# Optimization experiments

Hardware: AMD Instinct MI355X
Metric: run time of the kernel (lower is better)

## Reference

```python
import jax, jax.numpy as jnp
import numpy as np

D = 1024        # hidden_dim
E = 8           # num_experts
K = 2           # activated_experts
H = 4 * D       # ffn hidden


def setup_inputs() -> dict:
    key = jax.random.key(0)
    ks = jax.random.split(key, 12)
    s = 1.0 / np.sqrt(D)
    sh = 1.0 / np.sqrt(H)
    return {
        "x": jax.random.normal(ks[0], (2, 2048, D), dtype=jnp.float32),
        "gate_w": jax.random.uniform(ks[1], (D, E), minval=-s, maxval=s, dtype=jnp.float32),
        "gate_b": jax.random.uniform(ks[2], (E,), minval=-s, maxval=s, dtype=jnp.float32),
        "route_bias": jnp.zeros((E,), dtype=jnp.float32),
        "shared_w1": jax.random.uniform(ks[3], (D, H), minval=-s, maxval=s, dtype=jnp.float32),
        "shared_b1": jax.random.uniform(ks[4], (H,), minval=-s, maxval=s, dtype=jnp.float32),
        "shared_w2": jax.random.uniform(ks[5], (H, D), minval=-sh, maxval=sh, dtype=jnp.float32),
        "shared_b2": jax.random.uniform(ks[6], (D,), minval=-sh, maxval=sh, dtype=jnp.float32),
        "exp_w1": jax.random.uniform(ks[7], (E, D, H), minval=-s, maxval=s, dtype=jnp.float32),
        "exp_b1": jax.random.uniform(ks[8], (E, H), minval=-s, maxval=s, dtype=jnp.float32),
        "exp_w2": jax.random.uniform(ks[9], (E, H, D), minval=-sh, maxval=sh, dtype=jnp.float32),
        "exp_b2": jax.random.uniform(ks[10], (E, D), minval=-sh, maxval=sh, dtype=jnp.float32),
    }


def reference(x, gate_w, gate_b, route_bias, shared_w1, shared_b1, shared_w2,
              shared_b2, exp_w1, exp_b1, exp_w2, exp_b2):
    B, S, _ = x.shape
    xf = x.reshape(-1, D)                                  # [T, D]
    T = xf.shape[0]

    # Routing: gate logits + learned load-balancing bias -> softmax -> top-k
    gate_logits = xf @ gate_w + gate_b + route_bias        # [T, E]
    gate_probs = jax.nn.softmax(gate_logits, axis=-1)
    topk_p, topk_i = jax.lax.top_k(gate_probs, K)          # [T, K]
    topk_p = topk_p / jnp.sum(topk_p, axis=-1, keepdims=True)

    # Per-token combine weights over experts (zero for unselected experts)
    w = jnp.zeros((T, E), dtype=xf.dtype)
    w = w.at[jnp.arange(T)[:, None], topk_i].add(topk_p)   # [T, E]

    # Dense per-expert FFN (grouped GEMM form), weighted combine
    h = jax.nn.gelu(jnp.einsum('td,edh->eth', xf, exp_w1) + exp_b1[:, None, :],
                    approximate=False)                     # [E, T, H]
    y = jnp.einsum('eth,ehd->etd', h, exp_w2) + exp_b2[:, None, :]  # [E, T, D]
    combined = jnp.einsum('etd,te->td', y, w)              # [T, D]

    # Shared expert
    sh = jax.nn.gelu(xf @ shared_w1 + shared_b1, approximate=False)
    shared_out = sh @ shared_w2 + shared_b2                # [T, D]

    return (shared_out + combined).reshape(B, S, D)
```

## Files before the change

kernel.cpp:

```cpp
#include <hip/hip_runtime.h>
#include <math.h>

#define TT 4096
#define DD 1024
#define EE 8
#define HH 4096
#define NEXP 9

typedef __bf16 bf16;
typedef __bf16 bf16x8 __attribute__((ext_vector_type(8)));
typedef float  f32x4  __attribute__((ext_vector_type(4)));

#define GLOAD_LDS16(gptr, lptr)                                                   \
  __builtin_amdgcn_global_load_lds(                                               \
      (const __attribute__((address_space(1))) void*)(gptr),                      \
      (__attribute__((address_space(3))) void*)(lptr), 16, 0, 0)

__global__ void k_init(const float* __restrict__ x, bf16* __restrict__ xb,
                       float* __restrict__ out, int* __restrict__ counts,
                       int* __restrict__ cursors) {
  int i = blockIdx.x * blockDim.x + threadIdx.x;
  if (i < TT * DD) { xb[i] = (bf16)x[i]; out[i] = 0.0f; }
  if (i < EE) { counts[i] = 0; cursors[i] = 0; }
}

__global__ void k_route(const float* __restrict__ x, const float* __restrict__ gw,
                        const float* __restrict__ gb, const float* __restrict__ rb,
                        int* __restrict__ counts, int* __restrict__ tke,
                        float* __restrict__ tkp) {
  int gid = blockIdx.x * blockDim.x + threadIdx.x;
  int t = gid >> 6;
  int lane = gid & 63;
  if (t >= TT) return;
  const float* xt = x + (size_t)t * DD;
  float acc[EE];
#pragma unroll
  for (int e = 0; e < EE; e++) acc[e] = 0.f;
  for (int d = lane; d < DD; d += 64) {
    float xv = xt[d];
    const float* g = gw + (size_t)d * EE;
#pragma unroll
    for (int e = 0; e < EE; e++) acc[e] += xv * g[e];
  }
#pragma unroll
  for (int off = 32; off > 0; off >>= 1) {
#pragma unroll
    for (int e = 0; e < EE; e++) acc[e] += __shfl_down(acc[e], off);
  }
  if (lane == 0) {
    float l[EE];
#pragma unroll
    for (int e = 0; e < EE; e++) l[e] = acc[e] + gb[e] + rb[e];
    int i1 = 0;
#pragma unroll
    for (int e = 1; e < EE; e++) if (l[e] > l[i1]) i1 = e;
    int i2 = (i1 == 0) ? 1 : 0;
#pragma unroll
    for (int e = 0; e < EE; e++) if (e != i1 && l[e] > l[i2]) i2 = e;
    float e2 = expf(l[i2] - l[i1]);
    float s = 1.f + e2;
    tke[t * 2 + 0] = i1; tkp[t * 2 + 0] = 1.f / s;
    tke[t * 2 + 1] = i2; tkp[t * 2 + 1] = e2 / s;
    atomicAdd(&counts[i1], 1);
    atomicAdd(&counts[i2], 1);
  }
}

__global__ void k_prefix(const int* __restrict__ counts, int* __restrict__ expBase,
                         int* __restrict__ expCnt) {
  if (blockIdx.x == 0 && threadIdx.x == 0) {
    int off = TT;
    for (int e = 0; e < EE; e++) { expBase[e] = off; expCnt[e] = counts[e]; off += counts[e]; }
    expBase[8] = 0; expCnt[8] = TT;
  }
}

__global__ void k_scatter(const int* __restrict__ tke, const float* __restrict__ tkp,
                          const int* __restrict__ expBase, int* __restrict__ cursors,
                          int* __restrict__ rowTok, float* __restrict__ rowW) {
  int t = blockIdx.x * blockDim.x + threadIdx.x;
  if (t >= TT) return;
  rowTok[t] = t; rowW[t] = 1.f;
#pragma unroll
  for (int k = 0; k < 2; k++) {
    int e = tke[t * 2 + k];
    float p = tkp[t * 2 + k];
    int slot = atomicAdd(&cursors[e], 1);
    int r = expBase[e] + slot;
    rowTok[r] = t; rowW[r] = p;
  }
}

__global__ __launch_bounds__(256) void k_wt(const float* __restrict__ expW,
                                            const float* __restrict__ shW,
                                            bf16* __restrict__ outT, int K, int N) {
  __shared__ float t[64][65];
  int z = blockIdx.z;
  const float* W = (z == 8) ? shW : expW + (size_t)z * K * N;
  bf16* O = outT + (size_t)z * K * N;
  int n0 = blockIdx.x * 64, k0 = blockIdx.y * 64;
  int tid = threadIdx.x;
  int kr = tid >> 2;
  int cf = (tid & 3) * 16;
#pragma unroll
  for (int i = 0; i < 4; i++) {
    f32x4 v = *(const f32x4*)&W[(size_t)(k0 + kr) * N + n0 + cf + i * 4];
    t[kr][cf + i * 4 + 0] = v[0];
    t[kr][cf + i * 4 + 1] = v[1];
    t[kr][cf + i * 4 + 2] = v[2];
    t[kr][cf + i * 4 + 3] = v[3];
  }
  __syncthreads();
  int nr = tid >> 2;
  int kf = (tid & 3) * 16;
  bf16x8 o0, o1;
#pragma unroll
  for (int j = 0; j < 8; j++) o0[j] = (bf16)t[kf + j][nr];
#pragma unroll
  for (int j = 0; j < 8; j++) o1[j] = (bf16)t[kf + 8 + j][nr];
  bf16* dst = O + (size_t)(n0 + nr) * K + k0 + kf;
  *(bf16x8*)dst = o0;
  *(bf16x8*)(dst + 8) = o1;
}

__global__ __launch_bounds__(256, 2) void k_gemm1(
    const bf16* __restrict__ xb, const bf16* __restrict__ wt1,
    const float* __restrict__ sb1, const float* __restrict__ eb1,
    const int* __restrict__ rowTok, const int* __restrict__ expBase,
    const int* __restrict__ expCnt, bf16* __restrict__ hbuf) {
  int ex = blockIdx.z;
  int base = expBase[ex];
  int cnt  = expCnt[ex];
  int mt = blockIdx.y;
  if (mt * 128 >= cnt) return;
  int n0 = blockIdx.x * 128;
  const bf16* Bt = wt1 + (size_t)ex * HH * DD;
  const float* b1 = (ex == 8) ? sb1 : eb1 + (size_t)ex * HH;

  __shared__ bf16 As[128 * 32];
  __shared__ bf16 Bs[128 * 32];
  __shared__ int  toks[128];

  int tid = threadIdx.x;
  int lane = tid & 63;
  int wv = tid >> 6;
  int wm = (wv & 1) * 64;
  int wn = (wv >> 1) * 64;

  if (tid < 128) {
    int rr = min(mt * 128 + tid, cnt - 1);
    toks[tid] = rowTok[base + rr];
  }

  f32x4 acc[4][4];
#pragma unroll
  for (int a = 0; a < 4; a++)
#pragma unroll
    for (int b = 0; b < 4; b++) acc[a][b] = (f32x4){0.f, 0.f, 0.f, 0.f};

  __syncthreads();

  int r0 = wv * 32 + (lane >> 2);
  int c8 = (lane & 3) * 8;

  for (int k0 = 0; k0 < DD; k0 += 32) {
    GLOAD_LDS16(xb + (size_t)toks[r0] * DD + k0 + c8,      As + wv * 1024);
    GLOAD_LDS16(xb + (size_t)toks[r0 + 16] * DD + k0 + c8, As + wv * 1024 + 512);
    GLOAD_LDS16(Bt + (size_t)(n0 + r0) * DD + k0 + c8,      Bs + wv * 1024);
    GLOAD_LDS16(Bt + (size_t)(n0 + r0 + 16) * DD + k0 + c8, Bs + wv * 1024 + 512);
    __syncthreads();
    bf16x8 af[4], bfr[4];
#pragma unroll
    for (int mi = 0; mi < 4; mi++)
      af[mi] = *(const bf16x8*)&As[(wm + mi * 16 + (lane & 15)) * 32 + (lane >> 4) * 8];
#pragma unroll
    for (int ni = 0; ni < 4; ni++)
      bfr[ni] = *(const bf16x8*)&Bs[(wn + ni * 16 + (lane & 15)) * 32 + (lane >> 4) * 8];
#pragma unroll
    for (int mi = 0; mi < 4; mi++)
#pragma unroll
      for (int ni = 0; ni < 4; ni++)
        acc[mi][ni] = __builtin_amdgcn_mfma_f32_16x16x32_bf16(af[mi], bfr[ni], acc[mi][ni], 0, 0, 0);
    __syncthreads();
  }

  int rsub = (lane >> 4) * 4;
#pragma unroll
  for (int ni = 0; ni < 4; ni++) {
    int col = n0 + wn + ni * 16 + (lane & 15);
    float bias = b1[col];
#pragma unroll
    for (int mi = 0; mi < 4; mi++) {
#pragma unroll
      for (int r = 0; r < 4; r++) {
        int mrow = mt * 128 + wm + mi * 16 + rsub + r;
        if (mrow < cnt) {
          float v = acc[mi][ni][r] + bias;
          v = 0.5f * v * (1.f + erff(v * 0.70710678118654752f));
          hbuf[(size_t)(base + mrow) * HH + col] = (bf16)v;
        }
      }
    }
  }
}

__global__ __launch_bounds__(256, 2) void k_gemm2(
    const bf16* __restrict__ hbuf, const bf16* __restrict__ wt2,
    const float* __restrict__ sb2, const float* __restrict__ eb2,
    const int* __restrict__ rowTok, const float* __restrict__ rowW,
    const int* __restrict__ expBase, const int* __restrict__ expCnt,
    float* __restrict__ out) {
  int ex = blockIdx.z;
  int base = expBase[ex];
  int cnt  = expCnt[ex];
  int ks = blockIdx.y & 1;
  int mt = blockIdx.y >> 1;
  if (mt * 128 >= cnt) return;
  int n0 = blockIdx.x * 128;
  const bf16* Bt = wt2 + (size_t)ex * DD * HH;
  const float* b2 = (ex == 8) ? sb2 : eb2 + (size_t)ex * DD;

  __shared__ bf16 As[128 * 32];
  __shared__ bf16 Bs[128 * 32];
  __shared__ int   toks[128];
  __shared__ float wrow[128];

  int tid = threadIdx.x;
  int lane = tid & 63;
  int wv = tid >> 6;
  int wm = (wv & 1) * 64;
  int wn = (wv >> 1) * 64;

  if (tid < 128) {
    int rr = min(mt * 128 + tid, cnt - 1);
    toks[tid] = rowTok[base + rr];
    wrow[tid] = rowW[base + rr];
  }

  f32x4 acc[4][4];
#pragma unroll
  for (int a = 0; a < 4; a++)
#pragma unroll
    for (int b = 0; b < 4; b++) acc[a][b] = (f32x4){0.f, 0.f, 0.f, 0.f};

  __syncthreads();

  int r0 = wv * 32 + (lane >> 2);
  int c8 = (lane & 3) * 8;
  int pr0 = base + min(mt * 128 + r0, cnt - 1);
  int pr1 = base + min(mt * 128 + r0 + 16, cnt - 1);
  const bf16* ga0 = hbuf + (size_t)pr0 * HH + c8;
  const bf16* ga1 = hbuf + (size_t)pr1 * HH + c8;

  int kbeg = ks * (HH / 2), kend = kbeg + (HH / 2);
  for (int k0 = kbeg; k0 < kend; k0 += 32) {
    GLOAD_LDS16(ga0 + k0, As + wv * 1024);
    GLOAD_LDS16(ga1 + k0, As + wv * 1024 + 512);
    GLOAD_LDS16(Bt + (size_t)(n0 + r0) * HH + k0 + c8,      Bs + wv * 1024);
    GLOAD_LDS16(Bt + (size_t)(n0 + r0 + 16) * HH + k0 + c8, Bs + wv * 1024 + 512);
    __syncthreads();
    bf16x8 af[4], bfr[4];
#pragma unroll
    for (int mi = 0; mi < 4; mi++)
      af[mi] = *(const bf16x8*)&As[(wm + mi * 16 + (lane & 15)) * 32 + (lane >> 4) * 8];
#pragma unroll
    for (int ni = 0; ni < 4; ni++)
      bfr[ni] = *(const bf16x8*)&Bs[(wn + ni * 16 + (lane & 15)) * 32 + (lane >> 4) * 8];
#pragma unroll
    for (int mi = 0; mi < 4; mi++)
#pragma unroll
      for (int ni = 0; ni < 4; ni++)
        acc[mi][ni] = __builtin_amdgcn_mfma_f32_16x16x32_bf16(af[mi], bfr[ni], acc[mi][ni], 0, 0, 0);
    __syncthreads();
  }

  int rsub = (lane >> 4) * 4;
#pragma unroll
  for (int ni = 0; ni < 4; ni++) {
    int col = n0 + wn + ni * 16 + (lane & 15);
    float bias = (ks == 0) ? b2[col] : 0.f;
#pragma unroll
    for (int mi = 0; mi < 4; mi++) {
#pragma unroll
      for (int r = 0; r < 4; r++) {
        int local = wm + mi * 16 + rsub + r;
        int mrow = mt * 128 + local;
        if (mrow < cnt) {
          float v = acc[mi][ni][r] + bias;
          atomicAdd(&out[(size_t)toks[local] * DD + col], wrow[local] * v);
        }
      }
    }
  }
}

extern "C" void kernel_launch(void* const* d_in, const int* in_sizes, int n_in,
                              void* d_out, int out_size, void* d_ws, size_t ws_size,
                              hipStream_t stream) {
  const float* x   = (const float*)d_in[0];
  const float* gw  = (const float*)d_in[1];
  const float* gb  = (const float*)d_in[2];
  const float* rb  = (const float*)d_in[3];
  const float* sw1 = (const float*)d_in[4];
  const float* sb1 = (const float*)d_in[5];
  const float* sw2 = (const float*)d_in[6];
  const float* sb2 = (const float*)d_in[7];
  const float* ew1 = (const float*)d_in[8];
  const float* eb1 = (const float*)d_in[9];
  const float* ew2 = (const float*)d_in[10];
  const float* eb2 = (const float*)d_in[11];
  float* out = (float*)d_out;

  char* p = (char*)d_ws;
  bf16* xb    = (bf16*)p;  p += (size_t)TT * DD * sizeof(bf16);
  bf16* hbuf  = (bf16*)p;  p += (size_t)(3 * TT) * HH * sizeof(bf16);
  bf16* wtb   = (bf16*)p;  p += (size_t)NEXP * DD * HH * sizeof(bf16);
  int* rowTok = (int*)p;   p += (size_t)(3 * TT) * sizeof(int);
  float* rowW = (float*)p; p += (size_t)(3 * TT) * sizeof(float);
  int* tke    = (int*)p;   p += (size_t)TT * 2 * sizeof(int);
  float* tkp  = (float*)p; p += (size_t)TT * 2 * sizeof(float);
  int* counts = (int*)p;   p += EE * sizeof(int);
  int* cursors= (int*)p;   p += EE * sizeof(int);
  int* expBase= (int*)p;   p += NEXP * sizeof(int);
  int* expCnt = (int*)p;   p += NEXP * sizeof(int);

  k_init<<<(TT * DD + 255) / 256, 256, 0, stream>>>(x, xb, out, counts, cursors);
  k_route<<<TT / 4, 256, 0, stream>>>(x, gw, gb, rb, counts, tke, tkp);
  k_prefix<<<1, 64, 0, stream>>>(counts, expBase, expCnt);
  k_scatter<<<TT / 256, 256, 0, stream>>>(tke, tkp, expBase, cursors, rowTok, rowW);

  dim3 gt1(HH / 64, DD / 64, NEXP);
  k_wt<<<gt1, 256, 0, stream>>>(ew1, sw1, wtb, DD, HH);
  dim3 g1(HH / 128, 32, NEXP);
  k_gemm1<<<g1, 256, 0, stream>>>(xb, wtb, sb1, eb1, rowTok, expBase, expCnt, hbuf);

  dim3 gt2(DD / 64, HH / 64, NEXP);
  k_wt<<<gt2, 256, 0, stream>>>(ew2, sw2, wtb, HH, DD);
  dim3 g2(DD / 128, 64, NEXP);
  k_gemm2<<<g2, 256, 0, stream>>>(hbuf, wtb, sb2, eb2, rowTok, rowW, expBase, expCnt, out);
}
```

Baseline: 919.9 us.

## Use compact tile list with grouped raster order for MoE GEMMs, drop split-K

Builds a compact list of (expert, m-tile) work items in the prefix kernel so both GEMMs launch only useful blocks instead of a 3D grid with many early-exit blocks. Blocks are rasterised in groups of 8 m-tiles per n-column to improve L2 reuse of weight tiles. GEMM2 also drops its 2-way split-K and runs the full K loop per block, halving the atomic adds to the output but giving fewer blocks and longer per-block work.

```diff
diff --git a/kernel.cpp b/kernel.cpp
--- a/kernel.cpp
+++ b/kernel.cpp
@@ -6,6 +6,8 @@
 #define EE 8
 #define HH 4096
 #define NEXP 9
+#define NTMAX 104
+#define NSG 13
 
 typedef __bf16 bf16;
 typedef __bf16 bf16x8 __attribute__((ext_vector_type(8)));
@@ -67,11 +69,19 @@
 }
 
 __global__ void k_prefix(const int* __restrict__ counts, int* __restrict__ expBase,
-                         int* __restrict__ expCnt) {
+                         int* __restrict__ expCnt, int* __restrict__ tileExp,
+                         int* __restrict__ tileM, int* __restrict__ nTiles) {
   if (blockIdx.x == 0 && threadIdx.x == 0) {
     int off = TT;
     for (int e = 0; e < EE; e++) { expBase[e] = off; expCnt[e] = counts[e]; off += counts[e]; }
     expBase[8] = 0; expCnt[8] = TT;
+    int idx = 0;
+    for (int mt = 0; mt < TT / 128; mt++) { tileExp[idx] = 8; tileM[idx] = mt; idx++; }
+    for (int e = 0; e < EE; e++) {
+      int nt = (counts[e] + 127) >> 7;
+      for (int mt = 0; mt < nt; mt++) { tileExp[idx] = e; tileM[idx] = mt; idx++; }
+    }
+    *nTiles = idx;
   }
 }
 
@@ -127,13 +137,21 @@
     const bf16* __restrict__ xb, const bf16* __restrict__ wt1,
     const float* __restrict__ sb1, const float* __restrict__ eb1,
     const int* __restrict__ rowTok, const int* __restrict__ expBase,
-    const int* __restrict__ expCnt, bf16* __restrict__ hbuf) {
-  int ex = blockIdx.z;
+    const int* __restrict__ expCnt, const int* __restrict__ tileExp,
+    const int* __restrict__ tileM, const int* __restrict__ nTiles,
+    bf16* __restrict__ hbuf) {
+  int bid = blockIdx.x;
+  int sg  = bid >> 8;
+  int rem = bid & 255;
+  int n   = rem >> 3;
+  int dm  = rem & 7;
+  int tIdx = sg * 8 + dm;
+  if (tIdx >= *nTiles) return;
+  int ex = tileExp[tIdx];
+  int mt = tileM[tIdx];
   int base = expBase[ex];
   int cnt  = expCnt[ex];
-  int mt = blockIdx.y;
-  if (mt * 128 >= cnt) return;
-  int n0 = blockIdx.x * 128;
+  int n0 = n * 128;
   const bf16* Bt = wt1 + (size_t)ex * HH * DD;
   const float* b1 = (ex == 8) ? sb1 : eb1 + (size_t)ex * HH;
 
@@ -209,14 +227,20 @@
     const float* __restrict__ sb2, const float* __restrict__ eb2,
     const int* __restrict__ rowTok, const float* __restrict__ rowW,
     const int* __restrict__ expBase, const int* __restrict__ expCnt,
-    float* __restrict__ out) {
-  int ex = blockIdx.z;
+    const int* __restrict__ tileExp, const int* __restrict__ tileM,
+    const int* __restrict__ nTiles, float* __restrict__ out) {
+  int bid = blockIdx.x;
+  int sg  = bid >> 6;
+  int rem = bid & 63;
+  int n   = rem >> 3;
+  int dm  = rem & 7;
+  int tIdx = sg * 8 + dm;
+  if (tIdx >= *nTiles) return;
+  int ex = tileExp[tIdx];
+  int mt = tileM[tIdx];
   int base = expBase[ex];
   int cnt  = expCnt[ex];
-  int ks = blockIdx.y & 1;
-  int mt = blockIdx.y >> 1;
-  if (mt * 128 >= cnt) return;
-  int n0 = blockIdx.x * 128;
+  int n0 = n * 128;
   const bf16* Bt = wt2 + (size_t)ex * DD * HH;
   const float* b2 = (ex == 8) ? sb2 : eb2 + (size_t)ex * DD;
 
@@ -252,8 +276,7 @@
   const bf16* ga0 = hbuf + (size_t)pr0 * HH + c8;
   const bf16* ga1 = hbuf + (size_t)pr1 * HH + c8;
 
-  int kbeg = ks * (HH / 2), kend = kbeg + (HH / 2);
-  for (int k0 = kbeg; k0 < kend; k0 += 32) {
+  for (int k0 = 0; k0 < HH; k0 += 32) {
     GLOAD_LDS16(ga0 + k0, As + wv * 1024);
     GLOAD_LDS16(ga1 + k0, As + wv * 1024 + 512);
     GLOAD_LDS16(Bt + (size_t)(n0 + r0) * HH + k0 + c8,      Bs + wv * 1024);
@@ -278,7 +301,7 @@
 #pragma unroll
   for (int ni = 0; ni < 4; ni++) {
     int col = n0 + wn + ni * 16 + (lane & 15);
-    float bias = (ks == 0) ? b2[col] : 0.f;
+    float bias = b2[col];
 #pragma unroll
     for (int mi = 0; mi < 4; mi++) {
 #pragma unroll
@@ -323,19 +346,22 @@
   int* cursors= (int*)p;   p += EE * sizeof(int);
   int* expBase= (int*)p;   p += NEXP * sizeof(int);
   int* expCnt = (int*)p;   p += NEXP * sizeof(int);
+  int* tileExp= (int*)p;   p += 128 * sizeof(int);
+  int* tileM  = (int*)p;   p += 128 * sizeof(int);
+  int* nTiles = (int*)p;   p += 8 * sizeof(int);
 
   k_init<<<(TT * DD + 255) / 256, 256, 0, stream>>>(x, xb, out, counts, cursors);
   k_route<<<TT / 4, 256, 0, stream>>>(x, gw, gb, rb, counts, tke, tkp);
-  k_prefix<<<1, 64, 0, stream>>>(counts, expBase, expCnt);
+  k_prefix<<<1, 64, 0, stream>>>(counts, expBase, expCnt, tileExp, tileM, nTiles);
   k_scatter<<<TT / 256, 256, 0, stream>>>(tke, tkp, expBase, cursors, rowTok, rowW);
 
   dim3 gt1(HH / 64, DD / 64, NEXP);
   k_wt<<<gt1, 256, 0, stream>>>(ew1, sw1, wtb, DD, HH);
-  dim3 g1(HH / 128, 32, NEXP);
-  k_gemm1<<<g1, 256, 0, stream>>>(xb, wtb, sb1, eb1, rowTok, expBase, expCnt, hbuf);
+  k_gemm1<<<NSG * 8 * (HH / 128), 256, 0, stream>>>(xb, wtb, sb1, eb1, rowTok, expBase,
+                                                    expCnt, tileExp, tileM, nTiles, hbuf);
 
   dim3 gt2(DD / 64, HH / 64, NEXP);
   k_wt<<<gt2, 256, 0, stream>>>(ew2, sw2, wtb, HH, DD);
-  dim3 g2(DD / 128, 64, NEXP);
-  k_gemm2<<<g2, 256, 0, stream>>>(hbuf, wtb, sb2, eb2, rowTok, rowW, expBase, expCnt, out);
-}
+  k_gemm2<<<NSG * 8 * (DD / 128), 256, 0, stream>>>(hbuf, wtb, sb2, eb2, rowTok, rowW,
+                                                    expBase, expCnt, tileExp, tileM, nTiles, out);
+}
```

Measured after the change: 904.5 us. No clear change (-1.7%).
